# Performance work log

Measured on AMD Instinct MI355X. Metric: run time of the kernel, lower is better.

Reference implementation:

```python
import jax, jax.numpy as jnp
import numpy as np

VOCAB, EMB, FILT, HID, WIN = 32000, 256, 256, 256, 3
B, S = 64, 1024
T = S - WIN + 1  # conv 'valid' output length = 1022


def setup_inputs() -> dict:
    key = jax.random.key(0)
    ks = jax.random.split(key, 12)
    inp = {}
    inp['ipts'] = jax.random.randint(ks[0], (B, S), 0, VOCAB, dtype=jnp.int64 if jax.config.jax_enable_x64 else jnp.int32)
    inp['seq_lengths'] = jax.random.randint(ks[1], (B,), 1, T + 1, dtype=jnp.int32)
    inp['h0'] = jnp.zeros((1, B, HID), jnp.float32)
    inp['c0'] = jnp.zeros((1, B, HID), jnp.float32)
    # learned params
    inp['emb'] = jax.random.normal(ks[2], (VOCAB, EMB), jnp.float32) * 0.1
    inp['emb'] = inp['emb'].at[0].set(0.0)  # padding_idx=0
    inp['conv_w'] = jax.random.normal(ks[3], (WIN, EMB, FILT), jnp.float32) * 0.05  # WIO layout
    inp['conv_b'] = jnp.zeros((FILT,), jnp.float32)
    inp['w_ih'] = jax.random.normal(ks[4], (4 * HID, FILT), jnp.float32) * 0.05  # gate order i,f,g,o
    inp['w_hh'] = jax.random.normal(ks[5], (4 * HID, HID), jnp.float32) * 0.05
    inp['b_ih'] = jnp.zeros((4 * HID,), jnp.float32)
    inp['b_hh'] = jnp.zeros((4 * HID,), jnp.float32)
    inp['lin_w'] = jax.random.normal(ks[6], (1, HID), jnp.float32) * 0.05
    inp['lin_b'] = jnp.zeros((1,), jnp.float32)
    return inp


def reference(ipts, seq_lengths, h0, c0, emb, conv_w, conv_b, w_ih, w_hh, b_ih, b_hh, lin_w, lin_b):
    # Embedding: [B,S,E]
    x = emb[ipts]
    x = jax.lax.conv_general_dilated(x, conv_w, window_strides=(1,), padding='VALID',
                                     dimension_numbers=('NWC', 'WIO', 'NWC')) + conv_b
    # time-major for the RNN: [T,B,F]
    xt = jnp.transpose(x, (1, 0, 2))

    def step(carry, x_t):
        h, c = carry
        g = x_t @ w_ih.T + h @ w_hh.T + (b_ih + b_hh)
        i, f, gg, o = jnp.split(g, 4, axis=-1)
        c = jax.nn.sigmoid(f) * c + jax.nn.sigmoid(i) * jnp.tanh(gg)
        h = jax.nn.sigmoid(o) * jnp.tanh(c)
        return (h, c), h

    _, hs = jax.lax.scan(step, (h0[0], c0[0]), xt)  # hs: [T,B,H]

    # masked mean over real lengths (dropout is identity at eval).
    t = hs.shape[0]
    mask = (jnp.arange(t)[:, None] < seq_lengths[None, :]).astype(hs.dtype)  # [T,B]
    mot = jnp.einsum('tbh,tb->bh', hs, mask) / seq_lengths[:, None].astype(hs.dtype)  # [B,H]

    out = jax.nn.sigmoid(mot @ lin_w.T + lin_b)  # [B,1]
    return out.squeeze(-1)
```

## Files before the change

kernel.cpp:

```cpp
#include <hip/hip_runtime.h>
#include <hip/hip_bf16.h>
#include <math.h>

#define TLEN 1022
#define SLEN 1024
#define NB   64
#define NE   256
#define NF   256
#define NH   256
#define NG   1024
#define TC   256
#define CQL  8

typedef _Float16 h2_t __attribute__((ext_vector_type(2)));
typedef __attribute__((ext_vector_type(8))) short bf16x8;
typedef __attribute__((ext_vector_type(4))) float f32x4;

#if defined(__has_builtin)
# if __has_builtin(__builtin_amdgcn_sdot4)
#  define HAVE_SDOT4 1
# endif
#endif
#ifndef HAVE_SDOT4
# define HAVE_SDOT4 0
#endif

__device__ __forceinline__ float sigm(float x){ return 1.f/(1.f+__expf(-x)); }
__device__ __forceinline__ float tanh_(float x){ return 1.f - 2.f/(__expf(2.f*x)+1.f); }

__device__ __forceinline__ int sdot4_acc(unsigned int a, unsigned int b, int acc){
#if HAVE_SDOT4
  return __builtin_amdgcn_sdot4((int)a, (int)b, acc, false);
#else
  int s = acc;
  #pragma unroll
  for (int e=0;e<4;++e){
    int av = (int)(signed char)((a >> (8*e)) & 0xff);
    int bv = (int)(signed char)((b >> (8*e)) & 0xff);
    s += av*bv;
  }
  return s;
#endif
}
__device__ __forceinline__ unsigned short f2bf(float x){
  __hip_bfloat16 b = __float2bfloat16(x);
  return __builtin_bit_cast(unsigned short, b);
}

__global__ __launch_bounds__(256) void k_bias(const float* __restrict__ conv_b,
                                              const float* __restrict__ w_ih,
                                              const float* __restrict__ b_ih,
                                              const float* __restrict__ b_hh,
                                              float* __restrict__ bias4){
  int g = blockIdx.x*256 + threadIdx.x;
  const float* row = w_ih + (size_t)g*NF;
  float s = b_ih[g] + b_hh[g];
  for (int f=0; f<NF; f+=4){
    float4 w4 = *(const float4*)(row+f);
    float4 c4 = *(const float4*)(conv_b+f);
    s += w4.x*c4.x + w4.y*c4.y + w4.z*c4.z + w4.w*c4.w;
  }
  bias4[g] = s;
}

__global__ __launch_bounds__(256) void k_scale(const float* __restrict__ w_hh,
                                               float* __restrict__ stepv,
                                               float* __restrict__ sws){
  int row = blockIdx.x*256 + threadIdx.x;
  const float* p = w_hh + (size_t)row*NH;
  float m = 0.f;
  for (int c=0;c<NH;c+=4){
    float4 v = *(const float4*)(p+c);
    m = fmaxf(m, fmaxf(fmaxf(fabsf(v.x),fabsf(v.y)), fmaxf(fabsf(v.z),fabsf(v.w))));
  }
  float st = fmaxf(m, 1e-20f) / 127.f;
  stepv[row] = st;
  sws[row]   = st / 127.f;
}

__global__ __launch_bounds__(256) void k_pack3(const float* __restrict__ w_hh,
                                               const float* __restrict__ stepv,
                                               uint2* __restrict__ pq2){
  int gid = blockIdx.x*256 + threadIdx.x;
  int tid5 = gid & 511, rp = (gid>>9)&3, cq = gid>>11;
  int l = tid5 & 63, wv = tid5 >> 6, kq = wv >> 1, jh = wv & 1;
  unsigned int words[2];
  #pragma unroll
  for (int w2=0; w2<2; ++w2){
    int r = rp*2 + w2;
    int row = jh*512 + l*8 + r;
    float st = stepv[row];
    unsigned int acc = 0;
    #pragma unroll
    for (int e=0;e<4;++e){
      int col = kq*64 + cq*4 + e;
      int q = __float2int_rn(w_hh[(size_t)row*NH + col] / st);
      q = max(-127, min(127, q));
      acc |= ((unsigned int)(unsigned char)(signed char)q) << (8*e);
    }
    words[w2] = acc;
  }
  pq2[(size_t)(cq*4 + rp)*512 + tid5] = make_uint2(words[0], words[1]);
}

__global__ __launch_bounds__(256) void k_cw2(const float* __restrict__ w_ih,
                                             const float* __restrict__ conv_w,
                                             unsigned short* __restrict__ cw2t){
  __shared__ float al[64][17];
  __shared__ float bl[16][64];
  const int n0  = blockIdx.x*64;
  const int m0  = blockIdx.y*64;
  const int tid = threadIdx.x;
  const int ty  = tid>>4, tx = tid&15;
  const int rr  = tid>>2, kq = (tid&3)<<2;
  float acc[4][4];
  #pragma unroll
  for (int i=0;i<4;++i){ acc[i][0]=0.f; acc[i][1]=0.f; acc[i][2]=0.f; acc[i][3]=0.f; }

  for (int k0=0; k0<256; k0+=16){
    __syncthreads();
    {
      float4 v = *(const float4*)(w_ih + (size_t)(m0+rr)*NF + k0 + kq);
      al[rr][kq+0]=v.x; al[rr][kq+1]=v.y; al[rr][kq+2]=v.z; al[rr][kq+3]=v.w;
      float4 u = *(const float4*)(conv_w + (size_t)(n0+rr)*NF + k0 + kq);
      bl[kq+0][rr]=u.x; bl[kq+1][rr]=u.y; bl[kq+2][rr]=u.z; bl[kq+3][rr]=u.w;
    }
    __syncthreads();
    #pragma unroll
    for (int kk=0; kk<16; ++kk){
      float a0=al[ty*4+0][kk], a1=al[ty*4+1][kk], a2=al[ty*4+2][kk], a3=al[ty*4+3][kk];
      float4 bv = *(const float4*)&bl[kk][tx*4];
      acc[0][0]+=a0*bv.x; acc[0][1]+=a0*bv.y; acc[0][2]+=a0*bv.z; acc[0][3]+=a0*bv.w;
      acc[1][0]+=a1*bv.x; acc[1][1]+=a1*bv.y; acc[1][2]+=a1*bv.z; acc[1][3]+=a1*bv.w;
      acc[2][0]+=a2*bv.x; acc[2][1]+=a2*bv.y; acc[2][2]+=a2*bv.z; acc[2][3]+=a2*bv.w;
      acc[3][0]+=a3*bv.x; acc[3][1]+=a3*bv.y; acc[3][2]+=a3*bv.z; acc[3][3]+=a3*bv.w;
    }
  }
  #pragma unroll
  for (int i=0;i<4;++i){
    size_t r = (size_t)m0 + ty*4 + i;
    unsigned int p0 = (unsigned int)f2bf(acc[i][0]) | ((unsigned int)f2bf(acc[i][1])<<16);
    unsigned int p1 = (unsigned int)f2bf(acc[i][2]) | ((unsigned int)f2bf(acc[i][3])<<16);
    *(uint2*)(cw2t + r*768 + n0 + tx*4) = make_uint2(p0, p1);
  }
}

__global__ __launch_bounds__(256,2) void k_fxg(const int* __restrict__ ipts,
                                               const float* __restrict__ emb,
                                               const unsigned short* __restrict__ cw2t,
                                               const float* __restrict__ bias4,
                                               unsigned short* __restrict__ xh,
                                               int t0){
  __shared__ unsigned short A_l[128][72];
  __shared__ unsigned short B_l[256][72];
  __shared__ int tokl[4][64];
  const int tid = threadIdx.x;
  const int l   = tid & 63, wv = tid >> 6;
  const int m0  = blockIdx.x * 128;
  const int n0  = blockIdx.y * 256;
  const int TL0 = m0 >> 6;
  {
    int tv = tid >> 6, b = tid & 63;
    tokl[tv][b] = ipts[b*SLEN + t0 + TL0 + tv];
  }

  f32x4 acc[4][8];
  #pragma unroll
  for (int mt=0; mt<4; ++mt)
    #pragma unroll
    for (int nt=0; nt<8; ++nt)
      acc[mt][nt] = (f32x4){0.f,0.f,0.f,0.f};

  const int wm = wv >> 1, wn = wv & 1;
  const int lr = l & 15, lk = l >> 4;

  for (int ks = 0; ks < 12; ++ks){
    const int w0 = ks >> 2;
    const int e0 = (ks & 3) << 6;
    __syncthreads();
    #pragma unroll
    for (int s = 0; s < 4; ++s){
      int seg = tid + s*256;
      int row = seg >> 3, off = seg & 7;
      int tok = tokl[(row>>6) + w0][row & 63];
      const float* src = emb + (size_t)tok*NE + e0 + off*8;
      float4 f0 = *(const float4*)src;
      float4 f1 = *(const float4*)(src+4);
      unsigned int p0 = (unsigned int)f2bf(f0.x) | ((unsigned int)f2bf(f0.y)<<16);
      unsigned int p1 = (unsigned int)f2bf(f0.z) | ((unsigned int)f2bf(f0.w)<<16);
      unsigned int p2 = (unsigned int)f2bf(f1.x) | ((unsigned int)f2bf(f1.y)<<16);
      unsigned int p3 = (unsigned int)f2bf(f1.z) | ((unsigned int)f2bf(f1.w)<<16);
      *(uint4*)&A_l[row][off*8] = make_uint4(p0,p1,p2,p3);
    }
    #pragma unroll
    for (int s = 0; s < 8; ++s){
      int seg = tid + s*256;
      int row = seg >> 3, off = seg & 7;
      uint4 v = *(const uint4*)(cw2t + (size_t)(n0+row)*768 + (ks<<6) + off*8);
      *(uint4*)&B_l[row][off*8] = v;
    }
    __syncthreads();
    #pragma unroll
    for (int kf = 0; kf < 2; ++kf){
      bf16x8 af[4], bfr[8];
      #pragma unroll
      for (int mt=0; mt<4; ++mt)
        af[mt] = *(const bf16x8*)&A_l[wm*64 + mt*16 + lr][kf*32 + lk*8];
      #pragma unroll
      for (int nt=0; nt<8; ++nt)
        bfr[nt] = *(const bf16x8*)&B_l[wn*128 + nt*16 + lr][kf*32 + lk*8];
      #pragma unroll
      for (int mt=0; mt<4; ++mt)
        #pragma unroll
        for (int nt=0; nt<8; ++nt)
          acc[mt][nt] = __builtin_amdgcn_mfma_f32_16x16x32_bf16(af[mt], bfr[nt], acc[mt][nt], 0,0,0);
    }
  }

  float bia[8];
  #pragma unroll
  for (int nt=0; nt<8; ++nt) bia[nt] = bias4[n0 + wn*128 + nt*16 + lr];
  #pragma unroll
  for (int mt=0; mt<4; ++mt){
    #pragma unroll
    for (int nt=0; nt<8; ++nt){
      #pragma unroll
      for (int r=0; r<4; ++r){
        int row = m0 + wm*64 + mt*16 + lk*4 + r;
        int col = n0 + wn*128 + nt*16 + lr;
        _Float16 hv = (_Float16)(acc[mt][nt][r] + bia[nt]);
        xh[(size_t)row*NG + col] = __builtin_bit_cast(unsigned short, hv);
      }
    }
  }
}

__global__ __attribute__((amdgpu_flat_work_group_size(512,512)))
__attribute__((amdgpu_waves_per_eu(2,2)))
void k_rnn3(const unsigned short* __restrict__ xh,
            const uint2* __restrict__ pq2,
            const float* __restrict__ sws,
            const float* __restrict__ h0,
            const float* __restrict__ c0,
            const int* __restrict__ seqlen,
            const float* __restrict__ lin_w,
            const float* __restrict__ lin_b,
            float* __restrict__ h_ws,
            float* __restrict__ c_ws,
            float* __restrict__ ms_ws,
            float* __restrict__ out,
            int t0, int tcount, int is_first, int is_last){
  __shared__ uint2 wlds[CQL*4][512];
  __shared__ float part2[4][2][8][68];
  __shared__ unsigned int hq32[64];
  __shared__ float red[256];
  const int b   = blockIdx.x;
  const int tid = threadIdx.x;
  const int l   = tid & 63, wv = tid >> 6;
  const int kq  = wv >> 1, jh = wv & 1;
  const int jbase = jh*512 + l*8;

  #pragma unroll
  for (int i=0;i<CQL*4;++i) wlds[i][tid] = pq2[(size_t)i*512 + tid];

  unsigned int wreg[(16-CQL)*8];
  #pragma unroll
  for (int cq=CQL; cq<16; ++cq){
    #pragma unroll
    for (int rp=0; rp<4; ++rp){
      uint2 v = pq2[(size_t)(cq*4+rp)*512 + tid];
      wreg[(cq-CQL)*8 + rp*2 + 0] = v.x;
      wreg[(cq-CQL)*8 + rp*2 + 1] = v.y;
    }
  }
  #pragma unroll
  for (int i=0;i<(16-CQL)*8;++i) asm volatile("" : "+v"(wreg[i]));

  float swr[8];
  #pragma unroll
  for (int r=0;r<8;++r) swr[r] = sws[jbase + r];

  float creg = 0.f, msum = 0.f, hlast = 0.f;
  if (tid < 256){
    float hv;
    if (is_first){ hv = h0[(size_t)b*NH + tid]; creg = c0[(size_t)b*NH + tid]; }
    else { hv = h_ws[b*256 + tid]; creg = c_ws[b*256 + tid]; msum = ms_ws[b*256 + tid]; }
    hlast = hv;
    int q = __float2int_rn(hv * 127.f);
    q = max(-127, min(127, q));
    ((signed char*)hq32)[tid] = (signed char)q;
  }
  const int L = seqlen[b];
  __syncthreads();

  const unsigned short* xrow = xh + (size_t)b*NG + tid;

  for (int tl=0; tl<tcount; ++tl){
    unsigned short xr0=0, xr1=0, xr2=0, xr3=0;
    if (tid < 256){
      const unsigned short* xr = xrow + (size_t)tl*NB*NG;
      xr0 = xr[0]; xr1 = xr[256]; xr2 = xr[512]; xr3 = xr[768];
    }

    int pa[8];
    #pragma unroll
    for (int r=0;r<8;++r) pa[r]=0;

    #pragma unroll
    for (int cq=0; cq<16; ++cq){
      unsigned int hw = hq32[kq*16 + cq];
      if (cq < CQL){
        #pragma unroll
        for (int rp=0; rp<4; ++rp){
          uint2 wv2 = wlds[cq*4+rp][tid];
          pa[rp*2+0] = sdot4_acc(wv2.x, hw, pa[rp*2+0]);
          pa[rp*2+1] = sdot4_acc(wv2.y, hw, pa[rp*2+1]);
        }
      } else {
        #pragma unroll
        for (int r=0;r<8;++r)
          pa[r] = sdot4_acc(wreg[(cq-CQL)*8 + r], hw, pa[r]);
      }
    }

    #pragma unroll
    for (int r=0;r<8;++r) part2[kq][jh][r][l] = (float)pa[r] * swr[r];
    __syncthreads();

    if (tid < 256){
      unsigned short xr4[4] = {xr0, xr1, xr2, xr3};
      float a[4];
      #pragma unroll
      for (int q=0;q<4;++q){
        int G = q*256 + tid;
        int jh2 = G>>9, rw = G&511, l2 = rw>>3, r2 = rw&7;
        float s = (float)__builtin_bit_cast(_Float16, xr4[q]);
        #pragma unroll
        for (int k=0;k<4;++k) s += part2[k][jh2][r2][l2];
        a[q] = s;
      }
      float si = sigm(a[0]), sf = sigm(a[1]), so = sigm(a[3]);
      float tg = tanh_(a[2]);
      creg = sf*creg + si*tg;
      float h2 = so*tanh_(creg);
      if (t0 + tl < L) msum += h2;
      hlast = h2;
      int q2 = __float2int_rn(h2 * 127.f);
      q2 = max(-127, min(127, q2));
      ((signed char*)hq32)[tid] = (signed char)q2;
    }
    __syncthreads();
  }

  if (tid < 256){
    h_ws[b*256 + tid]  = hlast;
    c_ws[b*256 + tid]  = creg;
    ms_ws[b*256 + tid] = msum;
  }

  if (is_last){
    if (tid < 256) red[tid] = (msum / (float)L) * lin_w[tid];
    __syncthreads();
    if (tid < 64){
      float s = red[tid] + red[tid+64] + red[tid+128] + red[tid+192];
      #pragma unroll
      for (int off=32; off>0; off>>=1) s += __shfl_down(s, off);
      if (tid==0) out[b] = sigm(s + lin_b[0]);
    }
  }
}

extern "C" void kernel_launch(void* const* d_in, const int* in_sizes, int n_in,
                              void* d_out, int out_size, void* d_ws, size_t ws_size,
                              hipStream_t stream){
  const int*   ipts   = (const int*)d_in[0];
  const int*   seqlen = (const int*)d_in[1];
  const float* h0     = (const float*)d_in[2];
  const float* c0     = (const float*)d_in[3];
  const float* emb    = (const float*)d_in[4];
  const float* conv_w = (const float*)d_in[5];
  const float* conv_b = (const float*)d_in[6];
  const float* w_ih   = (const float*)d_in[7];
  const float* w_hh   = (const float*)d_in[8];
  const float* b_ih   = (const float*)d_in[9];
  const float* b_hh   = (const float*)d_in[10];
  const float* lin_w  = (const float*)d_in[11];
  const float* lin_b  = (const float*)d_in[12];
  float* out = (float*)d_out;

  char* ws = (char*)d_ws;
  const size_t XH_B   = (size_t)TC*NB*NG*2;
  const size_t CW2_B  = (size_t)NG*768*2;
  const size_t PQ_B   = (size_t)16*4*512*8;
  size_t off = 0;
  unsigned short* xh    = (unsigned short*)(ws + off); off += XH_B;
  unsigned short* cw2t  = (unsigned short*)(ws + off); off += CW2_B;
  uint2*          pq2   = (uint2*)(ws + off);          off += PQ_B;
  float*          stepv = (float*)(ws + off);          off += 4096;
  float*          sws   = (float*)(ws + off);          off += 4096;
  float*          bias4 = (float*)(ws + off);          off += 4096;
  float*          h_ws  = (float*)(ws + off);          off += 65536;
  float*          c_ws  = (float*)(ws + off);          off += 65536;
  float*          ms_ws = (float*)(ws + off);          off += 65536;

  k_bias <<<dim3(4),      dim3(256), 0, stream>>>(conv_b, w_ih, b_ih, b_hh, bias4);
  k_scale<<<dim3(4),      dim3(256), 0, stream>>>(w_hh, stepv, sws);
  k_pack3<<<dim3(128),    dim3(256), 0, stream>>>(w_hh, stepv, pq2);
  k_cw2  <<<dim3(12, 16), dim3(256), 0, stream>>>(w_ih, conv_w, cw2t);

  for (int t0 = 0; t0 < TLEN; t0 += TC){
    int tcount = (TLEN - t0 < TC) ? (TLEN - t0) : TC;
    int is_first = (t0 == 0), is_last = (t0 + TC >= TLEN);
    k_fxg <<<dim3(128, 4), dim3(256), 0, stream>>>(ipts, emb, cw2t, bias4, xh, t0);
    k_rnn3<<<dim3(NB),     dim3(512), 0, stream>>>(xh, pq2, sws, h0, c0, seqlen,
                                                   lin_w, lin_b, h_ws, c_ws, ms_ws, out,
                                                   t0, tcount, is_first, is_last);
  }
}
```

Baseline: 1.404 ms.

## Restructure LSTM recurrence so each thread owns a hidden unit's four gates

Recurrent weights are repacked so each thread holds all four gate rows of one hidden unit for half the K dimension. The two K halves are combined with a cross-lane shuffle instead of a shared-memory partial-sum buffer. This removes one of the two barriers per timestep and the separate gate-reduction phase, and a double-buffered h vector keeps the single barrier safe. Every thread now does the activation math redundantly with its partner lane, and the weights stay split between LDS and registers with a different ratio, which raises register pressure.

```diff
diff --git a/kernel.cpp b/kernel.cpp
--- a/kernel.cpp
+++ b/kernel.cpp
@@ -10,7 +10,6 @@
 #define NH   256
 #define NG   1024
 #define TC   256
-#define CQL  8
 
 typedef _Float16 h2_t __attribute__((ext_vector_type(2)));
 typedef __attribute__((ext_vector_type(8))) short bf16x8;
@@ -78,29 +77,31 @@
   sws[row]   = st / 127.f;
 }
 
-__global__ __launch_bounds__(256) void k_pack3(const float* __restrict__ w_hh,
+__global__ __launch_bounds__(256) void k_pack5(const float* __restrict__ w_hh,
                                                const float* __restrict__ stepv,
-                                               uint2* __restrict__ pq2){
+                                               uint2* __restrict__ pq5){
   int gid = blockIdx.x*256 + threadIdx.x;
-  int tid5 = gid & 511, rp = (gid>>9)&3, cq = gid>>11;
-  int l = tid5 & 63, wv = tid5 >> 6, kq = wv >> 1, jh = wv & 1;
+  int tid5 = gid & 511, slot = gid >> 9;
+  int g = slot >> 4, ip = slot & 15;
+  int w = tid5 >> 6, l = tid5 & 63;
+  int u = w*32 + (l & 31), kh = l >> 5;
+  int row = g*256 + u;
+  float st = stepv[row];
   unsigned int words[2];
   #pragma unroll
   for (int w2=0; w2<2; ++w2){
-    int r = rp*2 + w2;
-    int row = jh*512 + l*8 + r;
-    float st = stepv[row];
+    int i = ip*2 + w2;
     unsigned int acc = 0;
     #pragma unroll
-    for (int e=0;e<4;++e){
-      int col = kq*64 + cq*4 + e;
+    for (int e=0; e<4; ++e){
+      int col = kh*128 + i*4 + e;
       int q = __float2int_rn(w_hh[(size_t)row*NH + col] / st);
       q = max(-127, min(127, q));
       acc |= ((unsigned int)(unsigned char)(signed char)q) << (8*e);
     }
     words[w2] = acc;
   }
-  pq2[(size_t)(cq*4 + rp)*512 + tid5] = make_uint2(words[0], words[1]);
+  pq5[(size_t)slot*512 + tid5] = make_uint2(words[0], words[1]);
 }
 
 __global__ __launch_bounds__(256) void k_cw2(const float* __restrict__ w_ih,
@@ -237,8 +238,8 @@
 
 __global__ __attribute__((amdgpu_flat_work_group_size(512,512)))
 __attribute__((amdgpu_waves_per_eu(2,2)))
-void k_rnn3(const unsigned short* __restrict__ xh,
-            const uint2* __restrict__ pq2,
+void k_rnn5(const unsigned short* __restrict__ xh,
+            const uint2* __restrict__ pq5,
             const float* __restrict__ sws,
             const float* __restrict__ h0,
             const float* __restrict__ c0,
@@ -250,116 +251,101 @@
             float* __restrict__ ms_ws,
             float* __restrict__ out,
             int t0, int tcount, int is_first, int is_last){
-  __shared__ uint2 wlds[CQL*4][512];
-  __shared__ float part2[4][2][8][68];
-  __shared__ unsigned int hq32[64];
+  __shared__ uint2 wl2[24][512];
+  __shared__ unsigned int hbuf[2][64];
   __shared__ float red[256];
   const int b   = blockIdx.x;
   const int tid = threadIdx.x;
-  const int l   = tid & 63, wv = tid >> 6;
-  const int kq  = wv >> 1, jh = wv & 1;
-  const int jbase = jh*512 + l*8;
-
-  #pragma unroll
-  for (int i=0;i<CQL*4;++i) wlds[i][tid] = pq2[(size_t)i*512 + tid];
-
-  unsigned int wreg[(16-CQL)*8];
-  #pragma unroll
-  for (int cq=CQL; cq<16; ++cq){
-    #pragma unroll
-    for (int rp=0; rp<4; ++rp){
-      uint2 v = pq2[(size_t)(cq*4+rp)*512 + tid];
-      wreg[(cq-CQL)*8 + rp*2 + 0] = v.x;
-      wreg[(cq-CQL)*8 + rp*2 + 1] = v.y;
-    }
-  }
-  #pragma unroll
-  for (int i=0;i<(16-CQL)*8;++i) asm volatile("" : "+v"(wreg[i]));
-
-  float swr[8];
-  #pragma unroll
-  for (int r=0;r<8;++r) swr[r] = sws[jbase + r];
-
-  float creg = 0.f, msum = 0.f, hlast = 0.f;
-  if (tid < 256){
+  const int l   = tid & 63, w = tid >> 6;
+  const int u   = w*32 + (l & 31), kh = l >> 5;
+
+  #pragma unroll
+  for (int g=0; g<4; ++g)
+    #pragma unroll
+    for (int ip=0; ip<6; ++ip)
+      wl2[g*6+ip][tid] = pq5[(size_t)(g*16+ip)*512 + tid];
+
+  uint2 wr[4][10];
+  #pragma unroll
+  for (int g=0; g<4; ++g)
+    #pragma unroll
+    for (int ip=6; ip<16; ++ip)
+      wr[g][ip-6] = pq5[(size_t)(g*16+ip)*512 + tid];
+  #pragma unroll
+  for (int g=0; g<4; ++g)
+    #pragma unroll
+    for (int j=0; j<10; ++j)
+      asm volatile("" : "+v"(wr[g][j].x), "+v"(wr[g][j].y));
+
+  float swr[4];
+  #pragma unroll
+  for (int g=0; g<4; ++g) swr[g] = sws[g*256 + u];
+
+  const int L = seqlen[b];
+  float creg, msum, hlast;
+  {
     float hv;
-    if (is_first){ hv = h0[(size_t)b*NH + tid]; creg = c0[(size_t)b*NH + tid]; }
-    else { hv = h_ws[b*256 + tid]; creg = c_ws[b*256 + tid]; msum = ms_ws[b*256 + tid]; }
+    if (is_first){ hv = h0[(size_t)b*NH + u]; creg = c0[(size_t)b*NH + u]; msum = 0.f; }
+    else { hv = h_ws[b*256 + u]; creg = c_ws[b*256 + u]; msum = ms_ws[b*256 + u]; }
     hlast = hv;
-    int q = __float2int_rn(hv * 127.f);
-    q = max(-127, min(127, q));
-    ((signed char*)hq32)[tid] = (signed char)q;
-  }
-  const int L = seqlen[b];
+    int q = __float2int_rn(hv * 127.f); q = max(-127, min(127, q));
+    if (kh == 0) ((signed char*)&hbuf[0][0])[u] = (signed char)q;
+  }
   __syncthreads();
 
-  const unsigned short* xrow = xh + (size_t)b*NG + tid;
+  const unsigned short* xbase = xh + (size_t)b*NG + u;
 
   for (int tl=0; tl<tcount; ++tl){
-    unsigned short xr0=0, xr1=0, xr2=0, xr3=0;
-    if (tid < 256){
-      const unsigned short* xr = xrow + (size_t)tl*NB*NG;
-      xr0 = xr[0]; xr1 = xr[256]; xr2 = xr[512]; xr3 = xr[768];
-    }
-
-    int pa[8];
-    #pragma unroll
-    for (int r=0;r<8;++r) pa[r]=0;
-
-    #pragma unroll
-    for (int cq=0; cq<16; ++cq){
-      unsigned int hw = hq32[kq*16 + cq];
-      if (cq < CQL){
-        #pragma unroll
-        for (int rp=0; rp<4; ++rp){
-          uint2 wv2 = wlds[cq*4+rp][tid];
-          pa[rp*2+0] = sdot4_acc(wv2.x, hw, pa[rp*2+0]);
-          pa[rp*2+1] = sdot4_acc(wv2.y, hw, pa[rp*2+1]);
-        }
+    const int cur = tl & 1, nxt = cur ^ 1;
+
+    const unsigned short* xp = xbase + (size_t)tl*NB*NG;
+    unsigned short xr[4];
+    #pragma unroll
+    for (int g=0; g<4; ++g) xr[g] = xp[g*256];
+
+    int pa[4] = {0,0,0,0};
+    const unsigned int* hq = &hbuf[cur][kh*32];
+    #pragma unroll
+    for (int ip=0; ip<16; ++ip){
+      uint2 hw = *(const uint2*)&hq[ip*2];
+      uint2 w0, w1, w2, w3;
+      if (ip < 6){
+        w0 = wl2[0*6+ip][tid]; w1 = wl2[1*6+ip][tid];
+        w2 = wl2[2*6+ip][tid]; w3 = wl2[3*6+ip][tid];
       } else {
-        #pragma unroll
-        for (int r=0;r<8;++r)
-          pa[r] = sdot4_acc(wreg[(cq-CQL)*8 + r], hw, pa[r]);
+        w0 = wr[0][ip-6]; w1 = wr[1][ip-6]; w2 = wr[2][ip-6]; w3 = wr[3][ip-6];
       }
-    }
-
-    #pragma unroll
-    for (int r=0;r<8;++r) part2[kq][jh][r][l] = (float)pa[r] * swr[r];
-    __syncthreads();
-
-    if (tid < 256){
-      unsigned short xr4[4] = {xr0, xr1, xr2, xr3};
-      float a[4];
-      #pragma unroll
-      for (int q=0;q<4;++q){
-        int G = q*256 + tid;
-        int jh2 = G>>9, rw = G&511, l2 = rw>>3, r2 = rw&7;
-        float s = (float)__builtin_bit_cast(_Float16, xr4[q]);
-        #pragma unroll
-        for (int k=0;k<4;++k) s += part2[k][jh2][r2][l2];
-        a[q] = s;
-      }
-      float si = sigm(a[0]), sf = sigm(a[1]), so = sigm(a[3]);
-      float tg = tanh_(a[2]);
-      creg = sf*creg + si*tg;
-      float h2 = so*tanh_(creg);
-      if (t0 + tl < L) msum += h2;
-      hlast = h2;
-      int q2 = __float2int_rn(h2 * 127.f);
-      q2 = max(-127, min(127, q2));
-      ((signed char*)hq32)[tid] = (signed char)q2;
-    }
-    __syncthreads();
-  }
-
-  if (tid < 256){
-    h_ws[b*256 + tid]  = hlast;
-    c_ws[b*256 + tid]  = creg;
-    ms_ws[b*256 + tid] = msum;
+      pa[0] = sdot4_acc(w0.x, hw.x, pa[0]); pa[0] = sdot4_acc(w0.y, hw.y, pa[0]);
+      pa[1] = sdot4_acc(w1.x, hw.x, pa[1]); pa[1] = sdot4_acc(w1.y, hw.y, pa[1]);
+      pa[2] = sdot4_acc(w2.x, hw.x, pa[2]); pa[2] = sdot4_acc(w2.y, hw.y, pa[2]);
+      pa[3] = sdot4_acc(w3.x, hw.x, pa[3]); pa[3] = sdot4_acc(w3.y, hw.y, pa[3]);
+    }
+
+    float a[4];
+    #pragma unroll
+    for (int g=0; g<4; ++g){
+      int full = pa[g] + __shfl_xor(pa[g], 32, 64);
+      a[g] = (float)full * swr[g] + (float)__builtin_bit_cast(_Float16, xr[g]);
+    }
+    float si = sigm(a[0]), sf = sigm(a[1]), so = sigm(a[3]);
+    float tg = tanh_(a[2]);
+    creg = sf*creg + si*tg;
+    float h2 = so*tanh_(creg);
+    if (t0 + tl < L) msum += h2;
+    hlast = h2;
+    int q2 = __float2int_rn(h2 * 127.f); q2 = max(-127, min(127, q2));
+    if (kh == 0) ((signed char*)&hbuf[nxt][0])[u] = (signed char)q2;
+    __syncthreads();
+  }
+
+  if (kh == 0){
+    h_ws[b*256 + u]  = hlast;
+    c_ws[b*256 + u]  = creg;
+    ms_ws[b*256 + u] = msum;
   }
 
   if (is_last){
-    if (tid < 256) red[tid] = (msum / (float)L) * lin_w[tid];
+    if (kh == 0) red[u] = (msum / (float)L) * lin_w[u];
     __syncthreads();
     if (tid < 64){
       float s = red[tid] + red[tid+64] + red[tid+128] + red[tid+192];
@@ -391,11 +377,11 @@
   char* ws = (char*)d_ws;
   const size_t XH_B   = (size_t)TC*NB*NG*2;
   const size_t CW2_B  = (size_t)NG*768*2;
-  const size_t PQ_B   = (size_t)16*4*512*8;
+  const size_t PQ_B   = (size_t)64*512*8;
   size_t off = 0;
   unsigned short* xh    = (unsigned short*)(ws + off); off += XH_B;
   unsigned short* cw2t  = (unsigned short*)(ws + off); off += CW2_B;
-  uint2*          pq2   = (uint2*)(ws + off);          off += PQ_B;
+  uint2*          pq5   = (uint2*)(ws + off);          off += PQ_B;
   float*          stepv = (float*)(ws + off);          off += 4096;
   float*          sws   = (float*)(ws + off);          off += 4096;
   float*          bias4 = (float*)(ws + off);          off += 4096;
@@ -405,14 +391,14 @@
 
   k_bias <<<dim3(4),      dim3(256), 0, stream>>>(conv_b, w_ih, b_ih, b_hh, bias4);
   k_scale<<<dim3(4),      dim3(256), 0, stream>>>(w_hh, stepv, sws);
-  k_pack3<<<dim3(128),    dim3(256), 0, stream>>>(w_hh, stepv, pq2);
+  k_pack5<<<dim3(128),    dim3(256), 0, stream>>>(w_hh, stepv, pq5);
   k_cw2  <<<dim3(12, 16), dim3(256), 0, stream>>>(w_ih, conv_w, cw2t);
 
   for (int t0 = 0; t0 < TLEN; t0 += TC){
     int tcount = (TLEN - t0 < TC) ? (TLEN - t0) : TC;
     int is_first = (t0 == 0), is_last = (t0 + TC >= TLEN);
     k_fxg <<<dim3(128, 4), dim3(256), 0, stream>>>(ipts, emb, cw2t, bias4, xh, t0);
-    k_rnn3<<<dim3(NB),     dim3(512), 0, stream>>>(xh, pq2, sws, h0, c0, seqlen,
+    k_rnn5<<<dim3(NB),     dim3(512), 0, stream>>>(xh, pq5, sws, h0, c0, seqlen,
                                                    lin_w, lin_b, h_ws, c_ws, ms_ws, out,
                                                    t0, tcount, is_first, is_last);
   }
```

Result: no change. 1.409 ms (+0.4%).

## Split recurrent matvec over 1024 threads with 4 gate rows per thread

Applied to the files above, without the earlier changes.

The LSTM recurrence kernel now runs 1024 threads per batch block instead of 512. Each thread owns 4 gate rows rather than 8, and the int8 weights are repacked into uint4 words that are half held in LDS and half in registers. This halves the serial sdot4 chain each thread runs per timestep, which shortens the per-step critical path. The partial-sum layout in shared memory is also simplified to a row-contiguous float4 store. In exchange the kernel has more waves per block to synchronise, and register pressure rises under the waves_per_eu(4) constraint.

```diff
diff --git a/kernel.cpp b/kernel.cpp
--- a/kernel.cpp
+++ b/kernel.cpp
@@ -10,7 +10,6 @@
 #define NH   256
 #define NG   1024
 #define TC   256
-#define CQL  8
 
 typedef _Float16 h2_t __attribute__((ext_vector_type(2)));
 typedef __attribute__((ext_vector_type(8))) short bf16x8;
@@ -78,29 +77,28 @@
   sws[row]   = st / 127.f;
 }
 
-__global__ __launch_bounds__(256) void k_pack3(const float* __restrict__ w_hh,
+__global__ __launch_bounds__(256) void k_pack6(const float* __restrict__ w_hh,
                                                const float* __restrict__ stepv,
-                                               uint2* __restrict__ pq2){
+                                               uint4* __restrict__ pq6){
   int gid = blockIdx.x*256 + threadIdx.x;
-  int tid5 = gid & 511, rp = (gid>>9)&3, cq = gid>>11;
-  int l = tid5 & 63, wv = tid5 >> 6, kq = wv >> 1, jh = wv & 1;
-  unsigned int words[2];
-  #pragma unroll
-  for (int w2=0; w2<2; ++w2){
-    int r = rp*2 + w2;
-    int row = jh*512 + l*8 + r;
+  int i = gid >> 10, tid = gid & 1023;
+  int w = tid >> 6, l = tid & 63, kq = w >> 2, jq = w & 3;
+  unsigned int words[4];
+  #pragma unroll
+  for (int r=0; r<4; ++r){
+    int row = jq*256 + l*4 + r;
     float st = stepv[row];
     unsigned int acc = 0;
     #pragma unroll
-    for (int e=0;e<4;++e){
-      int col = kq*64 + cq*4 + e;
+    for (int e=0; e<4; ++e){
+      int col = kq*64 + i*4 + e;
       int q = __float2int_rn(w_hh[(size_t)row*NH + col] / st);
       q = max(-127, min(127, q));
       acc |= ((unsigned int)(unsigned char)(signed char)q) << (8*e);
     }
-    words[w2] = acc;
-  }
-  pq2[(size_t)(cq*4 + rp)*512 + tid5] = make_uint2(words[0], words[1]);
+    words[r] = acc;
+  }
+  pq6[(size_t)i*1024 + tid] = make_uint4(words[0],words[1],words[2],words[3]);
 }
 
 __global__ __launch_bounds__(256) void k_cw2(const float* __restrict__ w_ih,
@@ -235,10 +233,10 @@
   }
 }
 
-__global__ __attribute__((amdgpu_flat_work_group_size(512,512)))
-__attribute__((amdgpu_waves_per_eu(2,2)))
-void k_rnn3(const unsigned short* __restrict__ xh,
-            const uint2* __restrict__ pq2,
+__global__ __attribute__((amdgpu_flat_work_group_size(1024,1024)))
+__attribute__((amdgpu_waves_per_eu(4,4)))
+void k_rnn6(const unsigned short* __restrict__ xh,
+            const uint4* __restrict__ pq6,
             const float* __restrict__ sws,
             const float* __restrict__ h0,
             const float* __restrict__ c0,
@@ -250,47 +248,40 @@
             float* __restrict__ ms_ws,
             float* __restrict__ out,
             int t0, int tcount, int is_first, int is_last){
-  __shared__ uint2 wlds[CQL*4][512];
-  __shared__ float part2[4][2][8][68];
-  __shared__ unsigned int hq32[64];
+  __shared__ uint4 wlds[8][1024];
+  __shared__ float part[4][1024];
+  __shared__ unsigned int hq[64];
   __shared__ float red[256];
+  const int tid = threadIdx.x;
   const int b   = blockIdx.x;
-  const int tid = threadIdx.x;
-  const int l   = tid & 63, wv = tid >> 6;
-  const int kq  = wv >> 1, jh = wv & 1;
-  const int jbase = jh*512 + l*8;
-
-  #pragma unroll
-  for (int i=0;i<CQL*4;++i) wlds[i][tid] = pq2[(size_t)i*512 + tid];
-
-  unsigned int wreg[(16-CQL)*8];
-  #pragma unroll
-  for (int cq=CQL; cq<16; ++cq){
-    #pragma unroll
-    for (int rp=0; rp<4; ++rp){
-      uint2 v = pq2[(size_t)(cq*4+rp)*512 + tid];
-      wreg[(cq-CQL)*8 + rp*2 + 0] = v.x;
-      wreg[(cq-CQL)*8 + rp*2 + 1] = v.y;
-    }
-  }
-  #pragma unroll
-  for (int i=0;i<(16-CQL)*8;++i) asm volatile("" : "+v"(wreg[i]));
-
-  float swr[8];
-  #pragma unroll
-  for (int r=0;r<8;++r) swr[r] = sws[jbase + r];
-
+  const int l   = tid & 63, w = tid >> 6;
+  const int kq  = w >> 2, jq = w & 3;
+  const int rbase = jq*256 + l*4;
+
+  #pragma unroll
+  for (int i=0;i<8;++i) wlds[i][tid] = pq6[(size_t)i*1024 + tid];
+
+  uint4 wreg[8];
+  #pragma unroll
+  for (int i=8;i<16;++i) wreg[i-8] = pq6[(size_t)i*1024 + tid];
+  #pragma unroll
+  for (int i=0;i<8;++i)
+    asm volatile("" : "+v"(wreg[i].x), "+v"(wreg[i].y), "+v"(wreg[i].z), "+v"(wreg[i].w));
+
+  float swr[4];
+  #pragma unroll
+  for (int r=0;r<4;++r) swr[r] = sws[rbase + r];
+
+  const int L = seqlen[b];
   float creg = 0.f, msum = 0.f, hlast = 0.f;
   if (tid < 256){
     float hv;
     if (is_first){ hv = h0[(size_t)b*NH + tid]; creg = c0[(size_t)b*NH + tid]; }
     else { hv = h_ws[b*256 + tid]; creg = c_ws[b*256 + tid]; msum = ms_ws[b*256 + tid]; }
     hlast = hv;
-    int q = __float2int_rn(hv * 127.f);
-    q = max(-127, min(127, q));
-    ((signed char*)hq32)[tid] = (signed char)q;
-  }
-  const int L = seqlen[b];
+    int q = __float2int_rn(hv * 127.f); q = max(-127, min(127, q));
+    ((signed char*)hq)[tid] = (signed char)q;
+  }
   __syncthreads();
 
   const unsigned short* xrow = xh + (size_t)b*NG + tid;
@@ -302,42 +293,31 @@
       xr0 = xr[0]; xr1 = xr[256]; xr2 = xr[512]; xr3 = xr[768];
     }
 
-    int pa[8];
-    #pragma unroll
-    for (int r=0;r<8;++r) pa[r]=0;
-
-    #pragma unroll
-    for (int cq=0; cq<16; ++cq){
-      unsigned int hw = hq32[kq*16 + cq];
-      if (cq < CQL){
-        #pragma unroll
-        for (int rp=0; rp<4; ++rp){
-          uint2 wv2 = wlds[cq*4+rp][tid];
-          pa[rp*2+0] = sdot4_acc(wv2.x, hw, pa[rp*2+0]);
-          pa[rp*2+1] = sdot4_acc(wv2.y, hw, pa[rp*2+1]);
-        }
-      } else {
-        #pragma unroll
-        for (int r=0;r<8;++r)
-          pa[r] = sdot4_acc(wreg[(cq-CQL)*8 + r], hw, pa[r]);
-      }
-    }
-
-    #pragma unroll
-    for (int r=0;r<8;++r) part2[kq][jh][r][l] = (float)pa[r] * swr[r];
+    int pa[4] = {0,0,0,0};
+    #pragma unroll
+    for (int i=0;i<16;++i){
+      unsigned int hw = hq[kq*16 + i];
+      uint4 wv4 = (i < 8) ? wlds[i][tid] : wreg[i-8];
+      pa[0] = sdot4_acc(wv4.x, hw, pa[0]);
+      pa[1] = sdot4_acc(wv4.y, hw, pa[1]);
+      pa[2] = sdot4_acc(wv4.z, hw, pa[2]);
+      pa[3] = sdot4_acc(wv4.w, hw, pa[3]);
+    }
+    *(float4*)&part[kq][rbase & 1023] = make_float4(
+        (float)pa[0]*swr[0], (float)pa[1]*swr[1],
+        (float)pa[2]*swr[2], (float)pa[3]*swr[3]);
     __syncthreads();
 
     if (tid < 256){
       unsigned short xr4[4] = {xr0, xr1, xr2, xr3};
       float a[4];
       #pragma unroll
-      for (int q=0;q<4;++q){
-        int G = q*256 + tid;
-        int jh2 = G>>9, rw = G&511, l2 = rw>>3, r2 = rw&7;
-        float s = (float)__builtin_bit_cast(_Float16, xr4[q]);
+      for (int g=0; g<4; ++g){
+        float s = (float)__builtin_bit_cast(_Float16, xr4[g]);
+        int idx = g*256 + tid;
         #pragma unroll
-        for (int k=0;k<4;++k) s += part2[k][jh2][r2][l2];
-        a[q] = s;
+        for (int k=0;k<4;++k) s += part[k][idx];
+        a[g] = s;
       }
       float si = sigm(a[0]), sf = sigm(a[1]), so = sigm(a[3]);
       float tg = tanh_(a[2]);
@@ -345,9 +325,8 @@
       float h2 = so*tanh_(creg);
       if (t0 + tl < L) msum += h2;
       hlast = h2;
-      int q2 = __float2int_rn(h2 * 127.f);
-      q2 = max(-127, min(127, q2));
-      ((signed char*)hq32)[tid] = (signed char)q2;
+      int q2 = __float2int_rn(h2 * 127.f); q2 = max(-127, min(127, q2));
+      ((signed char*)hq)[tid] = (signed char)q2;
     }
     __syncthreads();
   }
@@ -391,11 +370,11 @@
   char* ws = (char*)d_ws;
   const size_t XH_B   = (size_t)TC*NB*NG*2;
   const size_t CW2_B  = (size_t)NG*768*2;
-  const size_t PQ_B   = (size_t)16*4*512*8;
+  const size_t PQ_B   = (size_t)16*1024*16;
   size_t off = 0;
   unsigned short* xh    = (unsigned short*)(ws + off); off += XH_B;
   unsigned short* cw2t  = (unsigned short*)(ws + off); off += CW2_B;
-  uint2*          pq2   = (uint2*)(ws + off);          off += PQ_B;
+  uint4*          pq6   = (uint4*)(ws + off);          off += PQ_B;
   float*          stepv = (float*)(ws + off);          off += 4096;
   float*          sws   = (float*)(ws + off);          off += 4096;
   float*          bias4 = (float*)(ws + off);          off += 4096;
@@ -405,15 +384,15 @@
 
   k_bias <<<dim3(4),      dim3(256), 0, stream>>>(conv_b, w_ih, b_ih, b_hh, bias4);
   k_scale<<<dim3(4),      dim3(256), 0, stream>>>(w_hh, stepv, sws);
-  k_pack3<<<dim3(128),    dim3(256), 0, stream>>>(w_hh, stepv, pq2);
+  k_pack6<<<dim3(64),     dim3(256), 0, stream>>>(w_hh, stepv, pq6);
   k_cw2  <<<dim3(12, 16), dim3(256), 0, stream>>>(w_ih, conv_w, cw2t);
 
   for (int t0 = 0; t0 < TLEN; t0 += TC){
     int tcount = (TLEN - t0 < TC) ? (TLEN - t0) : TC;
     int is_first = (t0 == 0), is_last = (t0 + TC >= TLEN);
-    k_fxg <<<dim3(128, 4), dim3(256), 0, stream>>>(ipts, emb, cw2t, bias4, xh, t0);
-    k_rnn3<<<dim3(NB),     dim3(512), 0, stream>>>(xh, pq2, sws, h0, c0, seqlen,
-                                                   lin_w, lin_b, h_ws, c_ws, ms_ws, out,
-                                                   t0, tcount, is_first, is_last);
-  }
-}
+    k_fxg <<<dim3(128, 4), dim3(256),  0, stream>>>(ipts, emb, cw2t, bias4, xh, t0);
+    k_rnn6<<<dim3(NB),     dim3(1024), 0, stream>>>(xh, pq6, sws, h0, c0, seqlen,
+                                                    lin_w, lin_b, h_ws, c_ws, ms_ws, out,
+                                                    t0, tcount, is_first, is_last);
+  }
+}
```

After: 1.259 ms. 10.3% less time.
